# Kernel optimization log

Hardware: AMD Instinct MI355X
Metric: run time of the kernel (lower is better)

The kernel has to match this reference:

```python
import jax, jax.numpy as jnp
import numpy as np
import math

B, S, E = 4, 2048, 1024

def setup_inputs() -> dict:
    key = jax.random.key(0)
    ks = jax.random.split(key, 12)
    scale = 1.0 / math.sqrt(E)
    inp = {
        "query": jax.random.normal(ks[0], (B, S, E), jnp.float32),
        "key_": jax.random.normal(ks[1], (B, S, E), jnp.float32),
        "value": jax.random.normal(ks[2], (B, S, E), jnp.float32),
        # causal mask, broadcast over batch: 1 = keep, 0 = mask
        "mask": jnp.broadcast_to(jnp.tril(jnp.ones((S, S), jnp.int32)), (B, S, S)),
        "Wq": jax.random.uniform(ks[3], (E, E), jnp.float32, -scale, scale),
        "bq": jax.random.uniform(ks[4], (E,), jnp.float32, -scale, scale),
        "Wk": jax.random.uniform(ks[5], (E, E), jnp.float32, -scale, scale),
        "bk": jax.random.uniform(ks[6], (E,), jnp.float32, -scale, scale),
        "Wv": jax.random.uniform(ks[7], (E, E), jnp.float32, -scale, scale),
        "bv": jax.random.uniform(ks[8], (E,), jnp.float32, -scale, scale),
        "Wo": jax.random.uniform(ks[9], (E, E), jnp.float32, -scale, scale),
        "bo": jax.random.uniform(ks[10], (E,), jnp.float32, -scale, scale),
    }
    return inp

def reference(query, key_, value, mask, Wq, bq, Wk, bk, Wv, bv, Wo, bo):
    # Linear projections (torch Linear: x @ W.T + b)
    Q = jnp.einsum('bse,fe->bsf', query, Wq) + bq
    K = jnp.einsum('bse,fe->bsf', key_, Wk) + bk
    V = jnp.einsum('bse,fe->bsf', value, Wv) + bv
    # NOTE: module never splits heads; scores over full embed_dim, scaled by sqrt(embed_dim)
    scores = jnp.einsum('bqe,bke->bqk', Q, K) / jnp.sqrt(jnp.asarray(E, Q.dtype))
    scores = jnp.where(mask == 0, -jnp.inf, scores)
    attn = jax.nn.softmax(scores, axis=-1)
    attn_out = jnp.einsum('bqk,bke->bqe', attn, V)
    return jnp.einsum('bse,fe->bsf', attn_out, Wo) + bo
```

## Files before the change

kernel.cpp:

```cpp
#include <hip/hip_runtime.h>

typedef __bf16 bf16;
typedef __attribute__((ext_vector_type(8))) __bf16 bf16x8;
typedef __attribute__((ext_vector_type(4))) __bf16 bf16x4;
typedef __attribute__((ext_vector_type(2))) __bf16 bf16x2;
typedef __attribute__((ext_vector_type(4))) float f32x4;

#define DEVINL __device__ __forceinline__

DEVINL void gload_lds16(const bf16* g, bf16* l) {
    __builtin_amdgcn_global_load_lds(
        (__attribute__((address_space(1))) unsigned int*)(unsigned long long)g,
        (__attribute__((address_space(3))) unsigned int*)l,
        16, 0, 0);
}

DEVINL void xcd_swizzle(int& bx, int& by) {
    const int gx = gridDim.x, gy = gridDim.y;
    const int l = blockIdx.y * gx + blockIdx.x;
    const int xcd = l & 7;
    const int li = l >> 3;
    by = xcd * (gy >> 3) + li / gx;
    bx = li - (li / gx) * gx;
}


__global__ __launch_bounds__(256) void cvt3_f32_to_bf16(
    const float* __restrict__ a, const float* __restrict__ b,
    const float* __restrict__ c, bf16* __restrict__ out, int n4) {
    int i = blockIdx.x * blockDim.x + threadIdx.x;
    if (i >= n4) return;
    const float* src = (blockIdx.z == 0) ? a : (blockIdx.z == 1) ? b : c;
    bf16* dst = out + (size_t)blockIdx.z * (size_t)n4 * 4;
    float4 f = ((const float4*)src)[i];
    bf16x4 o;
    o.x = (bf16)f.x; o.y = (bf16)f.y; o.z = (bf16)f.z; o.w = (bf16)f.w;
    ((bf16x4*)dst)[i] = o;
}

__global__ __launch_bounds__(256) void cvt4_f32_to_bf16(
    const float* __restrict__ a, const float* __restrict__ b,
    const float* __restrict__ c, const float* __restrict__ d,
    bf16* __restrict__ out, int n4) {
    int i = blockIdx.x * blockDim.x + threadIdx.x;
    if (i >= n4) return;
    const float* src = (blockIdx.z == 0) ? a : (blockIdx.z == 1) ? b
                     : (blockIdx.z == 2) ? c : d;
    bf16* dst = out + (size_t)blockIdx.z * (size_t)n4 * 4;
    float4 f = ((const float4*)src)[i];
    bf16x4 o;
    o.x = (bf16)f.x; o.y = (bf16)f.y; o.z = (bf16)f.z; o.w = (bf16)f.w;
    ((bf16x4*)dst)[i] = o;
}

__global__ __launch_bounds__(256) void transpose_bf16(
    const unsigned short* __restrict__ in, unsigned short* __restrict__ out,
    int R, int C) {
    __shared__ unsigned short t[64][65];
    const size_t bo = (size_t)blockIdx.z * R * C;
    const int r0 = blockIdx.y * 64, c0 = blockIdx.x * 64;
#pragma unroll
    for (int i = 0; i < 16; i++) {
        int lin = threadIdx.x + i * 256;
        int r = lin >> 6, c = lin & 63;
        t[r][c] = in[bo + (size_t)(r0 + r) * C + (c0 + c)];
    }
    __syncthreads();
#pragma unroll
    for (int i = 0; i < 16; i++) {
        int lin = threadIdx.x + i * 256;
        int r = lin >> 6, c = lin & 63;
        out[bo + (size_t)(c0 + r) * R + (r0 + c)] = t[c][r];
    }
}

template <int EPI>
__global__ __launch_bounds__(256) void gemm_bt128(
    const bf16* __restrict__ A, const bf16* __restrict__ B,
    const float* __restrict__ bias0, const float* __restrict__ bias1,
    const float* __restrict__ bias2, void* __restrict__ Cv,
    int M, int N, int K,
    long long sA, long long sB, long long sC,
    float scale) {
    int bx, by;
    xcd_swizzle(bx, by);
    const int bz = blockIdx.z;
    const int m0 = by * 128, n0 = bx * 128;

    A += (size_t)bz * sA;
    B += (size_t)bz * sB;
    const float* bias = (bz == 0) ? bias0 : (bz == 1) ? bias1 : bias2;

    __shared__ __align__(16) bf16 As[2][128 * 32];
    __shared__ __align__(16) bf16 Bs[2][128 * 32];

    const int tid = threadIdx.x;
    const int wave = tid >> 6;
    const int lane = tid & 63;
    const int lr = lane & 15;
    const int lq = lane >> 4;
    const int wm = (wave >> 1) * 64;
    const int wn = (wave & 1) * 64;
    const int srow = lane >> 2;
    const int scol = ((lane & 3) ^ ((lane >> 3) & 3)) * 8;

    const bf16* gA = A + (size_t)(m0 + wave * 16 + srow) * K + scol;
    const bf16* gB = B + (size_t)(n0 + wave * 16 + srow) * K + scol;
    const size_t rowskip = (size_t)64 * K;
    const int rsw = (lq ^ ((lr >> 1) & 3)) * 8;

    f32x4 acc[4][4];
    const f32x4 fzero = {0.f, 0.f, 0.f, 0.f};
#pragma unroll
    for (int i = 0; i < 4; i++)
#pragma unroll
        for (int j = 0; j < 4; j++) acc[i][j] = fzero;

#define STAGE128(bufi)                                        \
    do {                                                      \
        gload_lds16(gA,           As[bufi] + wave * 512);     \
        gload_lds16(gA + rowskip, As[bufi] + (wave + 4) * 512); \
        gload_lds16(gB,           Bs[bufi] + wave * 512);     \
        gload_lds16(gB + rowskip, Bs[bufi] + (wave + 4) * 512); \
        gA += 32; gB += 32;                                   \
    } while (0)

    STAGE128(0);
    int cur = 0;
    for (int k0 = 0; k0 < K; k0 += 32) {
        __syncthreads();
        if (k0 + 32 < K) STAGE128(cur ^ 1);

        bf16x8 af[4], bfr[4];
#pragma unroll
        for (int i = 0; i < 4; i++)
            af[i] = *(const bf16x8*)(As[cur] + (wm + i * 16 + lr) * 32 + rsw);
#pragma unroll
        for (int j = 0; j < 4; j++)
            bfr[j] = *(const bf16x8*)(Bs[cur] + (wn + j * 16 + lr) * 32 + rsw);
#pragma unroll
        for (int i = 0; i < 4; i++)
#pragma unroll
            for (int j = 0; j < 4; j++)
                acc[i][j] = __builtin_amdgcn_mfma_f32_16x16x32_bf16(
                    af[i], bfr[j], acc[i][j], 0, 0, 0);
        cur ^= 1;
    }
#undef STAGE128

#pragma unroll
    for (int j = 0; j < 4; j++) {
        const int col = n0 + wn + j * 16 + lr;
        const float bb = bias ? bias[col] : 0.0f;
#pragma unroll
        for (int i = 0; i < 4; i++) {
            const int rowb = m0 + wm + i * 16 + lq * 4;
#pragma unroll
            for (int r = 0; r < 4; r++) {
                if (EPI == 0)
                    ((bf16*)Cv)[(size_t)bz * sC + (size_t)(rowb + r) * N + col] =
                        (bf16)(acc[i][j][r] * scale + bb);
                else
                    ((float*)Cv)[(size_t)bz * sC + (size_t)(rowb + r) * N + col] =
                        acc[i][j][r] * scale + bb;
            }
        }
    }
}

template <int EPI>
__global__ __launch_bounds__(256) void gemm_bt64(
    const bf16* __restrict__ A, const bf16* __restrict__ B,
    const float* __restrict__ bias, void* __restrict__ Cv,
    int M, int N, int K,
    long long sA, long long sB, long long sC,
    float scale, int causal) {
    int bx, by;
    xcd_swizzle(bx, by);
    const int bz = blockIdx.z;
    const int m0 = by * 128, n0 = bx * 64;
    if (causal == 1 && n0 > m0 + 127) return;
    int Keff = K;
    if (causal == 2) { Keff = m0 + 128; if (Keff > K) Keff = K; }

    A += (size_t)bz * sA;
    B += (size_t)bz * sB;

    __shared__ __align__(16) bf16 As[2][128 * 32];
    __shared__ __align__(16) bf16 Bs[2][64 * 32];

    const int tid = threadIdx.x;
    const int wave = tid >> 6;
    const int lane = tid & 63;
    const int lr = lane & 15;
    const int lq = lane >> 4;
    const int wm = wave * 32;
    const int srow = lane >> 2;
    const int scol = ((lane & 3) ^ ((lane >> 3) & 3)) * 8;

    const bf16* gA = A + (size_t)(m0 + wave * 16 + srow) * K + scol;
    const bf16* gB = B + (size_t)(n0 + wave * 16 + srow) * K + scol;
    const size_t rowskip = (size_t)64 * K;
    const int rsw = (lq ^ ((lr >> 1) & 3)) * 8;

    f32x4 acc[2][4];
    const f32x4 fzero = {0.f, 0.f, 0.f, 0.f};
#pragma unroll
    for (int i = 0; i < 2; i++)
#pragma unroll
        for (int j = 0; j < 4; j++) acc[i][j] = fzero;

#define STAGE64(bufi)                                          \
    do {                                                       \
        gload_lds16(gA,           As[bufi] + wave * 512);      \
        gload_lds16(gA + rowskip, As[bufi] + (wave + 4) * 512); \
        gload_lds16(gB,           Bs[bufi] + wave * 512);      \
        gA += 32; gB += 32;                                    \
    } while (0)

    STAGE64(0);
    int cur = 0;
    for (int k0 = 0; k0 < Keff; k0 += 32) {
        __syncthreads();
        if (k0 + 32 < Keff) STAGE64(cur ^ 1);

        bf16x8 af[2], bfr[4];
#pragma unroll
        for (int i = 0; i < 2; i++)
            af[i] = *(const bf16x8*)(As[cur] + (wm + i * 16 + lr) * 32 + rsw);
#pragma unroll
        for (int j = 0; j < 4; j++)
            bfr[j] = *(const bf16x8*)(Bs[cur] + (j * 16 + lr) * 32 + rsw);
#pragma unroll
        for (int i = 0; i < 2; i++)
#pragma unroll
            for (int j = 0; j < 4; j++)
                acc[i][j] = __builtin_amdgcn_mfma_f32_16x16x32_bf16(
                    af[i], bfr[j], acc[i][j], 0, 0, 0);
        cur ^= 1;
    }
#undef STAGE64

#pragma unroll
    for (int j = 0; j < 4; j++) {
        const int col = n0 + j * 16 + lr;
        const float bb = bias ? bias[col] : 0.0f;
#pragma unroll
        for (int i = 0; i < 2; i++) {
            const int rowb = m0 + wm + i * 16 + lq * 4;
#pragma unroll
            for (int r = 0; r < 4; r++) {
                if (EPI == 0)
                    ((bf16*)Cv)[(size_t)bz * sC + (size_t)(rowb + r) * N + col] =
                        (bf16)(acc[i][j][r] * scale + bb);
                else
                    ((float*)Cv)[(size_t)bz * sC + (size_t)(rowb + r) * N + col] =
                        acc[i][j][r] * scale + bb;
            }
        }
    }
}

__global__ __launch_bounds__(256) void softmax_causal(
    const bf16* __restrict__ Sc, bf16* __restrict__ P, int S) {
    const int row = blockIdx.x;
    const int q = row & (S - 1);
    const bf16* src = Sc + (size_t)row * S;
    bf16* dst = P + (size_t)row * S;
    const int L = q + 1;
    const int tid = threadIdx.x;

    float v[8];
    float mx = -3.0e38f;
#pragma unroll
    for (int i = 0; i < 4; i++) {
        int k = (i * 256 + tid) * 2;
        bf16x2 u = ((const bf16x2*)src)[i * 256 + tid];
        v[2 * i]     = (k < L)     ? (float)u.x : -3.0e38f;
        v[2 * i + 1] = (k + 1 < L) ? (float)u.y : -3.0e38f;
        mx = fmaxf(mx, fmaxf(v[2 * i], v[2 * i + 1]));
    }
#pragma unroll
    for (int off = 32; off > 0; off >>= 1) mx = fmaxf(mx, __shfl_xor(mx, off, 64));
    __shared__ float redm[4], reds[4];
    if ((tid & 63) == 0) redm[tid >> 6] = mx;
    __syncthreads();
    mx = fmaxf(fmaxf(redm[0], redm[1]), fmaxf(redm[2], redm[3]));

    float sum = 0.f;
#pragma unroll
    for (int i = 0; i < 8; i++) {
        float e = (v[i] > -1.0e38f) ? __expf(v[i] - mx) : 0.f;
        v[i] = e;
        sum += e;
    }
#pragma unroll
    for (int off = 32; off > 0; off >>= 1) sum += __shfl_xor(sum, off, 64);
    if ((tid & 63) == 0) reds[tid >> 6] = sum;
    __syncthreads();
    sum = reds[0] + reds[1] + reds[2] + reds[3];
    const float inv = 1.0f / sum;
#pragma unroll
    for (int i = 0; i < 4; i++) {
        bf16x2 o;
        o.x = (bf16)(v[2 * i] * inv);
        o.y = (bf16)(v[2 * i + 1] * inv);
        ((bf16x2*)dst)[i * 256 + tid] = o;
    }
}

extern "C" void kernel_launch(void* const* d_in, const int* in_sizes, int n_in,
                              void* d_out, int out_size, void* d_ws, size_t ws_size,
                              hipStream_t stream) {
    const int B = 4, S = 2048, E = 1024;
    const size_t SBE = (size_t)B * S * E;
    const size_t EE = (size_t)E * E;

    const float* q_in = (const float*)d_in[0];
    const float* k_in = (const float*)d_in[1];
    const float* v_in = (const float*)d_in[2];
    const float* Wq = (const float*)d_in[4];
    const float* bq = (const float*)d_in[5];
    const float* Wk = (const float*)d_in[6];
    const float* bk = (const float*)d_in[7];
    const float* Wv = (const float*)d_in[8];
    const float* bv = (const float*)d_in[9];
    const float* Wo = (const float*)d_in[10];
    const float* bo = (const float*)d_in[11];

    char* ws = (char*)d_ws;
    bf16* qkvb = (bf16*)ws;
    bf16* Sc = (bf16*)ws;
    bf16* AO = (bf16*)ws;
    char* p = ws + (size_t)B * S * S * 4;
    bf16* QKVb = (bf16*)p; p += 3 * SBE * 2;
    bf16* Vt = (bf16*)p; p += SBE * 2;
    bf16* Pb = (bf16*)p; p += (size_t)B * S * S * 2;
    bf16* Wb = (bf16*)p; p += 4 * EE * 2;

    bf16* Qb = QKVb;
    bf16* Vb = QKVb + 2 * SBE;
    bf16* Wob = Wb + 3 * EE;

    dim3 gcvt3((int)(SBE / 4 / 256), 1, 3);
    cvt3_f32_to_bf16<<<gcvt3, 256, 0, stream>>>(q_in, k_in, v_in, qkvb, (int)(SBE / 4));
    dim3 gcvt4((int)(EE / 4 / 256), 1, 4);
    cvt4_f32_to_bf16<<<gcvt4, 256, 0, stream>>>(Wq, Wk, Wv, Wo, Wb, (int)(EE / 4));

    dim3 blk(256);
    dim3 gproj(E / 128, (B * S) / 128, 3);
    gemm_bt128<0><<<gproj, blk, 0, stream>>>(qkvb, Wb, bq, bk, bv, QKVb,
                                             B * S, E, E,
                                             (long long)SBE, (long long)EE,
                                             (long long)SBE, 1.f);

    dim3 gt(E / 64, S / 64, B);
    transpose_bf16<<<gt, blk, 0, stream>>>((const unsigned short*)Vb,
                                           (unsigned short*)Vt, S, E);

    dim3 gsc(S / 64, S / 128, B);
    gemm_bt64<0><<<gsc, blk, 0, stream>>>(Qb, QKVb + SBE, nullptr, Sc, S, S, E,
                                          (long long)S * E, (long long)S * E,
                                          (long long)S * S, 0.03125f, 1);

    softmax_causal<<<B * S, 256, 0, stream>>>(Sc, Pb, S);

    dim3 gpv(E / 64, S / 128, B);
    gemm_bt64<0><<<gpv, blk, 0, stream>>>(Pb, Vt, nullptr, AO, S, E, S,
                                          (long long)S * S, (long long)E * S,
                                          (long long)S * E, 1.f, 2);

    dim3 gout(E / 64, (B * S) / 128, 1);
    gemm_bt64<1><<<gout, blk, 0, stream>>>(AO, Wob, bo, (float*)d_out,
                                           B * S, E, E, 0, 0, 0, 1.f, 0);
}
```

Before: 419.3 us.

## Fold output projection into V projection and use register-fed 128x128 GEMMs

Precomputes Wo·Wv so the V projection directly yields V·Wvᵀ·Woᵀ, and folds Wo·bv + bo into a single output bias. This removes the final output-projection GEMM; the PV GEMM now writes fp32 output directly. The score and PV GEMMs switch from LDS-staged 128x64 tiles to 128x128 tiles that load fragments straight from global memory into registers with double buffering, plus a balanced XCD swizzle to even out causal work. It adds small weight-prep kernels, gives up LDS reuse in exchange for no syncs, and changes bf16 rounding because the weight product is formed in bf16.

Measured after the change: 533.4 us. 27.2% more time.

```diff
diff --git a/kernel.cpp b/kernel.cpp
--- a/kernel.cpp
+++ b/kernel.cpp
@@ -24,6 +24,15 @@
     bx = li - (li / gx) * gx;
 }
 
+DEVINL void xcd_swizzle_bal(int& bx, int& by) {
+    const int gx = gridDim.x, gy = gridDim.y;
+    const int l = blockIdx.y * gx + blockIdx.x;
+    const int xcd = l & 7;
+    const int li = l >> 3;
+    const int j = li / gx;
+    bx = li - j * gx;
+    by = j ? (gy - 1 - xcd) : xcd;
+}
 
 __global__ __launch_bounds__(256) void cvt3_f32_to_bf16(
     const float* __restrict__ a, const float* __restrict__ b,
@@ -74,6 +83,18 @@
     }
 }
 
+__global__ __launch_bounds__(256) void bias_fold(
+    const float* __restrict__ Wo, const float* __restrict__ bv,
+    const float* __restrict__ bo, float* __restrict__ bout) {
+    const int e = blockIdx.x * 4 + (threadIdx.x >> 6);
+    const int lane = threadIdx.x & 63;
+    float s = 0.f;
+    for (int k = lane; k < 1024; k += 64) s += Wo[e * 1024 + k] * bv[k];
+#pragma unroll
+    for (int off = 32; off > 0; off >>= 1) s += __shfl_xor(s, off, 64);
+    if (lane == 0) bout[e] = s + bo[e];
+}
+
 template <int EPI>
 __global__ __launch_bounds__(256) void gemm_bt128(
     const bf16* __restrict__ A, const bf16* __restrict__ B,
@@ -116,13 +137,13 @@
 #pragma unroll
         for (int j = 0; j < 4; j++) acc[i][j] = fzero;
 
-#define STAGE128(bufi)                                        \
-    do {                                                      \
-        gload_lds16(gA,           As[bufi] + wave * 512);     \
+#define STAGE128(bufi)                                          \
+    do {                                                        \
+        gload_lds16(gA,           As[bufi] + wave * 512);       \
         gload_lds16(gA + rowskip, As[bufi] + (wave + 4) * 512); \
-        gload_lds16(gB,           Bs[bufi] + wave * 512);     \
+        gload_lds16(gB,           Bs[bufi] + wave * 512);       \
         gload_lds16(gB + rowskip, Bs[bufi] + (wave + 4) * 512); \
-        gA += 32; gB += 32;                                   \
+        gA += 32; gB += 32;                                     \
     } while (0)
 
     STAGE128(0);
@@ -169,84 +190,72 @@
 }
 
 template <int EPI>
-__global__ __launch_bounds__(256) void gemm_bt64(
+__global__ __launch_bounds__(256) void gemm_reg(
     const bf16* __restrict__ A, const bf16* __restrict__ B,
     const float* __restrict__ bias, void* __restrict__ Cv,
     int M, int N, int K,
     long long sA, long long sB, long long sC,
     float scale, int causal) {
     int bx, by;
-    xcd_swizzle(bx, by);
+    xcd_swizzle_bal(bx, by);
     const int bz = blockIdx.z;
-    const int m0 = by * 128, n0 = bx * 64;
-    if (causal == 1 && n0 > m0 + 127) return;
+    const int m0 = by * 128, n0 = bx * 128;
+    if (causal == 1 && n0 > m0) return;
     int Keff = K;
     if (causal == 2) { Keff = m0 + 128; if (Keff > K) Keff = K; }
 
-    A += (size_t)bz * sA;
-    B += (size_t)bz * sB;
-
-    __shared__ __align__(16) bf16 As[2][128 * 32];
-    __shared__ __align__(16) bf16 Bs[2][64 * 32];
-
-    const int tid = threadIdx.x;
-    const int wave = tid >> 6;
-    const int lane = tid & 63;
+    const int lane = threadIdx.x & 63;
+    const int wave = threadIdx.x >> 6;
     const int lr = lane & 15;
     const int lq = lane >> 4;
-    const int wm = wave * 32;
-    const int srow = lane >> 2;
-    const int scol = ((lane & 3) ^ ((lane >> 3) & 3)) * 8;
-
-    const bf16* gA = A + (size_t)(m0 + wave * 16 + srow) * K + scol;
-    const bf16* gB = B + (size_t)(n0 + wave * 16 + srow) * K + scol;
-    const size_t rowskip = (size_t)64 * K;
-    const int rsw = (lq ^ ((lr >> 1) & 3)) * 8;
-
-    f32x4 acc[2][4];
+    const int wm = (wave >> 1) * 64;
+    const int wn = (wave & 1) * 64;
+
+    const bf16* pa = A + (size_t)bz * sA + (size_t)(m0 + wm + lr) * K + lq * 8;
+    const bf16* pb = B + (size_t)bz * sB + (size_t)(n0 + wn + lr) * K + lq * 8;
+    const size_t rs = (size_t)16 * K;
+
+    f32x4 acc[4][4];
     const f32x4 fzero = {0.f, 0.f, 0.f, 0.f};
 #pragma unroll
-    for (int i = 0; i < 2; i++)
+    for (int i = 0; i < 4; i++)
 #pragma unroll
         for (int j = 0; j < 4; j++) acc[i][j] = fzero;
 
-#define STAGE64(bufi)                                          \
-    do {                                                       \
-        gload_lds16(gA,           As[bufi] + wave * 512);      \
-        gload_lds16(gA + rowskip, As[bufi] + (wave + 4) * 512); \
-        gload_lds16(gB,           Bs[bufi] + wave * 512);      \
-        gA += 32; gB += 32;                                    \
+    bf16x8 a0[4], b0[4], a1[4], b1[4];
+
+#define LDFR(ar, br, koff)                                         \
+    do {                                                           \
+        _Pragma("unroll") for (int i = 0; i < 4; i++) {            \
+            ar[i] = *(const bf16x8*)(pa + (size_t)i * rs + (koff)); \
+            br[i] = *(const bf16x8*)(pb + (size_t)i * rs + (koff)); \
+        }                                                          \
     } while (0)
 
-    STAGE64(0);
-    int cur = 0;
-    for (int k0 = 0; k0 < Keff; k0 += 32) {
-        __syncthreads();
-        if (k0 + 32 < Keff) STAGE64(cur ^ 1);
-
-        bf16x8 af[2], bfr[4];
-#pragma unroll
-        for (int i = 0; i < 2; i++)
-            af[i] = *(const bf16x8*)(As[cur] + (wm + i * 16 + lr) * 32 + rsw);
-#pragma unroll
-        for (int j = 0; j < 4; j++)
-            bfr[j] = *(const bf16x8*)(Bs[cur] + (j * 16 + lr) * 32 + rsw);
-#pragma unroll
-        for (int i = 0; i < 2; i++)
-#pragma unroll
-            for (int j = 0; j < 4; j++)
-                acc[i][j] = __builtin_amdgcn_mfma_f32_16x16x32_bf16(
-                    af[i], bfr[j], acc[i][j], 0, 0, 0);
-        cur ^= 1;
-    }
-#undef STAGE64
+#define MF16(ar, br)                                               \
+    do {                                                           \
+        _Pragma("unroll") for (int i = 0; i < 4; i++)              \
+            _Pragma("unroll") for (int j = 0; j < 4; j++)          \
+                acc[i][j] = __builtin_amdgcn_mfma_f32_16x16x32_bf16( \
+                    ar[i], br[j], acc[i][j], 0, 0, 0);             \
+    } while (0)
+
+    LDFR(a0, b0, 0);
+    for (int k0 = 0; k0 < Keff; k0 += 64) {
+        LDFR(a1, b1, k0 + 32);
+        MF16(a0, b0);
+        if (k0 + 64 < Keff) LDFR(a0, b0, k0 + 64);
+        MF16(a1, b1);
+    }
+#undef LDFR
+#undef MF16
 
 #pragma unroll
     for (int j = 0; j < 4; j++) {
-        const int col = n0 + j * 16 + lr;
+        const int col = n0 + wn + j * 16 + lr;
         const float bb = bias ? bias[col] : 0.0f;
 #pragma unroll
-        for (int i = 0; i < 2; i++) {
+        for (int i = 0; i < 4; i++) {
             const int rowb = m0 + wm + i * 16 + lq * 4;
 #pragma unroll
             for (int r = 0; r < 4; r++) {
@@ -331,46 +340,54 @@
     char* ws = (char*)d_ws;
     bf16* qkvb = (bf16*)ws;
     bf16* Sc = (bf16*)ws;
-    bf16* AO = (bf16*)ws;
+    bf16* WvT = (bf16*)(ws + 3 * SBE * 2);
+    float* bout = (float*)(ws + 3 * SBE * 2 + EE * 2);
     char* p = ws + (size_t)B * S * S * 4;
     bf16* QKVb = (bf16*)p; p += 3 * SBE * 2;
-    bf16* Vt = (bf16*)p; p += SBE * 2;
+    bf16* VWt = (bf16*)p; p += SBE * 2;
     bf16* Pb = (bf16*)p; p += (size_t)B * S * S * 2;
     bf16* Wb = (bf16*)p; p += 4 * EE * 2;
 
     bf16* Qb = QKVb;
-    bf16* Vb = QKVb + 2 * SBE;
+    bf16* Kb = QKVb + SBE;
+    bf16* VW = QKVb + 2 * SBE;
     bf16* Wob = Wb + 3 * EE;
+    bf16* Wvo = Wb + 2 * EE;
+
+    dim3 blk(256);
 
     dim3 gcvt3((int)(SBE / 4 / 256), 1, 3);
-    cvt3_f32_to_bf16<<<gcvt3, 256, 0, stream>>>(q_in, k_in, v_in, qkvb, (int)(SBE / 4));
+    cvt3_f32_to_bf16<<<gcvt3, blk, 0, stream>>>(q_in, k_in, v_in, qkvb, (int)(SBE / 4));
     dim3 gcvt4((int)(EE / 4 / 256), 1, 4);
-    cvt4_f32_to_bf16<<<gcvt4, 256, 0, stream>>>(Wq, Wk, Wv, Wo, Wb, (int)(EE / 4));
-
-    dim3 blk(256);
+    cvt4_f32_to_bf16<<<gcvt4, blk, 0, stream>>>(Wq, Wk, Wv, Wo, Wb, (int)(EE / 4));
+
+    dim3 gtw(16, 16, 1);
+    transpose_bf16<<<gtw, blk, 0, stream>>>((const unsigned short*)(Wb + 2 * EE),
+                                            (unsigned short*)WvT, E, E);
+    dim3 gwvo(E / 128, E / 128, 1);
+    gemm_bt128<0><<<gwvo, blk, 0, stream>>>(Wob, WvT, nullptr, nullptr, nullptr,
+                                            Wvo, E, E, E, 0, 0, 0, 1.f);
+    bias_fold<<<256, blk, 0, stream>>>(Wo, bv, bo, bout);
+
     dim3 gproj(E / 128, (B * S) / 128, 3);
-    gemm_bt128<0><<<gproj, blk, 0, stream>>>(qkvb, Wb, bq, bk, bv, QKVb,
+    gemm_bt128<0><<<gproj, blk, 0, stream>>>(qkvb, Wb, bq, bk, nullptr, QKVb,
                                              B * S, E, E,
                                              (long long)SBE, (long long)EE,
                                              (long long)SBE, 1.f);
 
     dim3 gt(E / 64, S / 64, B);
-    transpose_bf16<<<gt, blk, 0, stream>>>((const unsigned short*)Vb,
-                                           (unsigned short*)Vt, S, E);
-
-    dim3 gsc(S / 64, S / 128, B);
-    gemm_bt64<0><<<gsc, blk, 0, stream>>>(Qb, QKVb + SBE, nullptr, Sc, S, S, E,
-                                          (long long)S * E, (long long)S * E,
-                                          (long long)S * S, 0.03125f, 1);
-
-    softmax_causal<<<B * S, 256, 0, stream>>>(Sc, Pb, S);
-
-    dim3 gpv(E / 64, S / 128, B);
-    gemm_bt64<0><<<gpv, blk, 0, stream>>>(Pb, Vt, nullptr, AO, S, E, S,
-                                          (long long)S * S, (long long)E * S,
-                                          (long long)S * E, 1.f, 2);
-
-    dim3 gout(E / 64, (B * S) / 128, 1);
-    gemm_bt64<1><<<gout, blk, 0, stream>>>(AO, Wob, bo, (float*)d_out,
-                                           B * S, E, E, 0, 0, 0, 1.f, 0);
-}
+    transpose_bf16<<<gt, blk, 0, stream>>>((const unsigned short*)VW,
+                                           (unsigned short*)VWt, S, E);
+
+    dim3 gsc(S / 128, S / 128, B);
+    gemm_reg<0><<<gsc, blk, 0, stream>>>(Qb, Kb, nullptr, Sc, S, S, E,
+                                         (long long)S * E, (long long)S * E,
+                                         (long long)S * S, 0.03125f, 1);
+
+    softmax_causal<<<B * S, blk, 0, stream>>>(Sc, Pb, S);
+
+    dim3 gpv(E / 128, S / 128, B);
+    gemm_reg<1><<<gpv, blk, 0, stream>>>(Pb, VWt, bout, (float*)d_out, S, E, S,
+                                         (long long)S * S, (long long)E * S,
+                                         (long long)S * E, 1.f, 2);
+}
```

## Fold output projection into V projection and balance causal tile scheduling

Applied to the files above, without the earlier changes.

Precomputes Wo·Wv as one fused weight and folds Wo·bv+bo into a single output bias. V is projected straight into the output space, so the PV GEMM writes the final float output and the separate output-projection GEMM goes away. It also adds a balanced XCD swizzle for the causal GEMMs that pairs short and long row tiles to even out per-XCD work. The cost is a small extra weight GEMM, a weight transpose and a bias reduction on every call, plus a different bf16 rounding path for the combined weight.

Measured after the change: 405.6 us. 3.3% less time.

```diff
diff --git a/kernel.cpp b/kernel.cpp
--- a/kernel.cpp
+++ b/kernel.cpp
@@ -24,6 +24,15 @@
     bx = li - (li / gx) * gx;
 }
 
+DEVINL void xcd_swizzle_bal(int& bx, int& by) {
+    const int gx = gridDim.x, gy = gridDim.y;
+    const int l = blockIdx.y * gx + blockIdx.x;
+    const int xcd = l & 7;
+    const int li = l >> 3;
+    const int j = li / gx;
+    bx = li - j * gx;
+    by = j ? (gy - 1 - xcd) : xcd;
+}
 
 __global__ __launch_bounds__(256) void cvt3_f32_to_bf16(
     const float* __restrict__ a, const float* __restrict__ b,
@@ -74,6 +83,18 @@
     }
 }
 
+__global__ __launch_bounds__(256) void bias_fold(
+    const float* __restrict__ Wo, const float* __restrict__ bv,
+    const float* __restrict__ bo, float* __restrict__ bout) {
+    const int e = blockIdx.x * 4 + (threadIdx.x >> 6);
+    const int lane = threadIdx.x & 63;
+    float s = 0.f;
+    for (int k = lane; k < 1024; k += 64) s += Wo[e * 1024 + k] * bv[k];
+#pragma unroll
+    for (int off = 32; off > 0; off >>= 1) s += __shfl_xor(s, off, 64);
+    if (lane == 0) bout[e] = s + bo[e];
+}
+
 template <int EPI>
 __global__ __launch_bounds__(256) void gemm_bt128(
     const bf16* __restrict__ A, const bf16* __restrict__ B,
@@ -116,13 +137,13 @@
 #pragma unroll
         for (int j = 0; j < 4; j++) acc[i][j] = fzero;
 
-#define STAGE128(bufi)                                        \
-    do {                                                      \
-        gload_lds16(gA,           As[bufi] + wave * 512);     \
+#define STAGE128(bufi)                                          \
+    do {                                                        \
+        gload_lds16(gA,           As[bufi] + wave * 512);       \
         gload_lds16(gA + rowskip, As[bufi] + (wave + 4) * 512); \
-        gload_lds16(gB,           Bs[bufi] + wave * 512);     \
+        gload_lds16(gB,           Bs[bufi] + wave * 512);       \
         gload_lds16(gB + rowskip, Bs[bufi] + (wave + 4) * 512); \
-        gA += 32; gB += 32;                                   \
+        gA += 32; gB += 32;                                     \
     } while (0)
 
     STAGE128(0);
@@ -176,7 +197,8 @@
     long long sA, long long sB, long long sC,
     float scale, int causal) {
     int bx, by;
-    xcd_swizzle(bx, by);
+    if (causal) xcd_swizzle_bal(bx, by);
+    else        xcd_swizzle(bx, by);
     const int bz = blockIdx.z;
     const int m0 = by * 128, n0 = bx * 64;
     if (causal == 1 && n0 > m0 + 127) return;
@@ -210,12 +232,12 @@
 #pragma unroll
         for (int j = 0; j < 4; j++) acc[i][j] = fzero;
 
-#define STAGE64(bufi)                                          \
-    do {                                                       \
-        gload_lds16(gA,           As[bufi] + wave * 512);      \
+#define STAGE64(bufi)                                           \
+    do {                                                        \
+        gload_lds16(gA,           As[bufi] + wave * 512);       \
         gload_lds16(gA + rowskip, As[bufi] + (wave + 4) * 512); \
-        gload_lds16(gB,           Bs[bufi] + wave * 512);      \
-        gA += 32; gB += 32;                                    \
+        gload_lds16(gB,           Bs[bufi] + wave * 512);       \
+        gA += 32; gB += 32;                                     \
     } while (0)
 
     STAGE64(0);
@@ -331,46 +353,54 @@
     char* ws = (char*)d_ws;
     bf16* qkvb = (bf16*)ws;
     bf16* Sc = (bf16*)ws;
-    bf16* AO = (bf16*)ws;
+    bf16* WvT = (bf16*)(ws + 3 * SBE * 2);
+    float* bout = (float*)(ws + 3 * SBE * 2 + EE * 2);
     char* p = ws + (size_t)B * S * S * 4;
     bf16* QKVb = (bf16*)p; p += 3 * SBE * 2;
-    bf16* Vt = (bf16*)p; p += SBE * 2;
+    bf16* VWt = (bf16*)p; p += SBE * 2;
     bf16* Pb = (bf16*)p; p += (size_t)B * S * S * 2;
     bf16* Wb = (bf16*)p; p += 4 * EE * 2;
 
     bf16* Qb = QKVb;
-    bf16* Vb = QKVb + 2 * SBE;
+    bf16* Kb = QKVb + SBE;
+    bf16* VW = QKVb + 2 * SBE;
     bf16* Wob = Wb + 3 * EE;
+    bf16* Wvo = Wb + 2 * EE;
+
+    dim3 blk(256);
 
     dim3 gcvt3((int)(SBE / 4 / 256), 1, 3);
-    cvt3_f32_to_bf16<<<gcvt3, 256, 0, stream>>>(q_in, k_in, v_in, qkvb, (int)(SBE / 4));
+    cvt3_f32_to_bf16<<<gcvt3, blk, 0, stream>>>(q_in, k_in, v_in, qkvb, (int)(SBE / 4));
     dim3 gcvt4((int)(EE / 4 / 256), 1, 4);
-    cvt4_f32_to_bf16<<<gcvt4, 256, 0, stream>>>(Wq, Wk, Wv, Wo, Wb, (int)(EE / 4));
-
-    dim3 blk(256);
+    cvt4_f32_to_bf16<<<gcvt4, blk, 0, stream>>>(Wq, Wk, Wv, Wo, Wb, (int)(EE / 4));
+
+    dim3 gtw(16, 16, 1);
+    transpose_bf16<<<gtw, blk, 0, stream>>>((const unsigned short*)(Wb + 2 * EE),
+                                            (unsigned short*)WvT, E, E);
+    dim3 gwvo(E / 128, E / 128, 1);
+    gemm_bt128<0><<<gwvo, blk, 0, stream>>>(Wob, WvT, nullptr, nullptr, nullptr,
+                                            Wvo, E, E, E, 0, 0, 0, 1.f);
+    bias_fold<<<256, blk, 0, stream>>>(Wo, bv, bo, bout);
+
     dim3 gproj(E / 128, (B * S) / 128, 3);
-    gemm_bt128<0><<<gproj, blk, 0, stream>>>(qkvb, Wb, bq, bk, bv, QKVb,
+    gemm_bt128<0><<<gproj, blk, 0, stream>>>(qkvb, Wb, bq, bk, nullptr, QKVb,
                                              B * S, E, E,
                                              (long long)SBE, (long long)EE,
                                              (long long)SBE, 1.f);
 
     dim3 gt(E / 64, S / 64, B);
-    transpose_bf16<<<gt, blk, 0, stream>>>((const unsigned short*)Vb,
-                                           (unsigned short*)Vt, S, E);
+    transpose_bf16<<<gt, blk, 0, stream>>>((const unsigned short*)VW,
+                                           (unsigned short*)VWt, S, E);
 
     dim3 gsc(S / 64, S / 128, B);
-    gemm_bt64<0><<<gsc, blk, 0, stream>>>(Qb, QKVb + SBE, nullptr, Sc, S, S, E,
+    gemm_bt64<0><<<gsc, blk, 0, stream>>>(Qb, Kb, nullptr, Sc, S, S, E,
                                           (long long)S * E, (long long)S * E,
                                           (long long)S * S, 0.03125f, 1);
 
-    softmax_causal<<<B * S, 256, 0, stream>>>(Sc, Pb, S);
+    softmax_causal<<<B * S, blk, 0, stream>>>(Sc, Pb, S);
 
     dim3 gpv(E / 64, S / 128, B);
-    gemm_bt64<0><<<gpv, blk, 0, stream>>>(Pb, Vt, nullptr, AO, S, E, S,
+    gemm_bt64<1><<<gpv, blk, 0, stream>>>(Pb, VWt, bout, (float*)d_out, S, E, S,
                                           (long long)S * S, (long long)E * S,
                                           (long long)S * E, 1.f, 2);
-
-    dim3 gout(E / 64, (B * S) / 128, 1);
-    gemm_bt64<1><<<gout, blk, 0, stream>>>(AO, Wob, bo, (float*)d_out,
-                                           B * S, E, E, 0, 0, 0, 1.f, 0);
-}
+}
```
